# Optimization experiments

Hardware: AMD Instinct MI355X
Metric: run time of the kernel (lower is better)

## Reference

```python
import jax, jax.numpy as jnp
import numpy as np

B, N, D, L = 32, 512, 768, 4  # batch, nodes (incl. CLS at last index), in_dim==hidden_size, num_layers


def setup_inputs() -> dict:
    key = jax.random.key(0)
    ks = jax.random.split(key, 6)
    feature = jax.random.normal(ks[0], (B, N, D), jnp.float32)
    # token mask: random valid lengths, CLS node at the last index always present
    lengths = jax.random.randint(ks[1], (B,), N // 2, N)
    pmask = (jnp.arange(N)[None, :] < lengths[:, None]).astype(jnp.float32)
    pmask = pmask.at[:, -1].set(1.0)
    # L2C (learning-to-connect) bilinear gate params, one pair per layer
    Wq = jax.random.normal(ks[2], (L, D, D), jnp.float32) / np.sqrt(D)
    Wk = jax.random.normal(ks[3], (L, D, D), jnp.float32) / np.sqrt(D)
    # attention-pool projection Linear(in_dim, 1)
    proj_w = jax.random.normal(ks[4], (D,), jnp.float32) / np.sqrt(D)
    proj_b = jnp.zeros((), jnp.float32)
    return dict(pmask=pmask, feature=feature, Wq=Wq, Wk=Wk, proj_w=proj_w, proj_b=proj_b)


def reference(pmask, feature, Wq, Wk, proj_w, proj_b):
    full_adj = pmask[:, :, None] * pmask[:, None, :]        # [B,N,N]
    full_sum = jnp.sum(full_adj) + 1e-8
    p_sum = pmask.sum(-1)                                    # [B]
    scale = 1.0 / np.sqrt(D)
    preds = [feature]
    adjs, c_list, g_list = [], [], []
    total_l0 = jnp.zeros((), feature.dtype)
    for l in range(L):
        # L2C: bilinear sigmoid gate masked by full adjacency, L0-style loss = mean gate mass
        q = jnp.einsum('bnd,de->bne', feature, Wq[l])
        k = jnp.einsum('bnd,de->bne', feature, Wk[l])
        adj = jax.nn.sigmoid(jnp.einsum('bne,bme->bnm', q, k) * scale) * full_adj  # [B,N,N]
        total_l0 = total_l0 + jnp.sum(adj) / full_sum
        # sparse_statistics: CLS-row sparsity and graph-edge sparsity
        c_list.append(adj[:, -1, :-1].sum(-1) / p_sum)               # [B]
        g_list.append(adj[:, :-1, :-1].sum((-1, -2)) / p_sum ** 2)   # [B]
        adjs.append(adj)
        # symmetric degree normalization: D^-1/2 A D^-1/2 (diag bmm == row/col scaling)
        deg = adj.sum(2)                                              # [B,N]
        dis = jnp.where(deg > 0, jax.lax.rsqrt(jnp.maximum(deg, 1e-12)), 0.0)
        dis = jax.lax.stop_gradient(dis)                              # .detach() in original
        adj_n = dis[:, :, None] * adj * dis[:, None, :]
        # feature = adj_^T @ feature
        feature = jnp.einsum('bnm,bnd->bmd', adj_n, feature)
        preds.append(feature)
    pps = jnp.stack(preds, axis=2)                                    # [B,N,L+1,D]
    retain = jax.nn.sigmoid(jnp.einsum('bnld,d->bnl', pps, proj_w) + proj_b)  # [B,N,L+1]
    out = jnp.einsum('bnl,bnld->bnd', retain, pps)                    # [B,N,D]
    c_sparsity = jnp.stack(c_list, axis=-1)                           # [B,L]
    g_sparsity = jnp.stack(g_list, axis=-1)                           # [B,L]
    return (out, retain, jnp.stack(adjs, axis=-1), total_l0 / L, c_sparsity, g_sparsity)
```

## Files before the change

### kernel.cpp

```cpp
#include <hip/hip_runtime.h>

typedef short s16x8 __attribute__((ext_vector_type(8)));
typedef float f32x4 __attribute__((ext_vector_type(4)));

constexpr int BATCH = 32, NODES = 512, DIM = 768, LAYERS = 4;
constexpr float QK_SCALE = 0.03608439182435161f;

constexpr size_t OUT_OFF  = 0;
constexpr size_t RET_OFF  = (size_t)BATCH * NODES * DIM;
constexpr size_t ADJS_OFF = RET_OFF + (size_t)BATCH * NODES * (LAYERS + 1);
constexpr size_t L0_OFF   = ADJS_OFF + (size_t)BATCH * NODES * NODES * LAYERS;
constexpr size_t C_OFF    = L0_OFF + 1;
constexpr size_t G_OFF    = C_OFF + BATCH * LAYERS;

#define DEVI static __device__ __forceinline__

DEVI float bf2f(unsigned short u) {
    union { unsigned int i; float f; } v; v.i = ((unsigned int)u) << 16; return v.f;
}
DEVI unsigned short f2bf(float f) {
    union { float f; unsigned int i; } v; v.f = f;
    return (unsigned short)((v.i + 0x7FFFu + ((v.i >> 16) & 1u)) >> 16);
}
DEVI ushort4 pk4(float4 v) {
    ushort4 o; o.x = f2bf(v.x); o.y = f2bf(v.y); o.z = f2bf(v.z); o.w = f2bf(v.w); return o;
}
DEVI float sigm(float x) { return 1.0f / (1.0f + __expf(-x)); }
DEVI float deg2dis(float d) { return d > 0.f ? rsqrtf(fmaxf(d, 1e-12f)) : 0.f; }

DEVI void gload16(const unsigned short* g, unsigned short* l) {
    __builtin_amdgcn_global_load_lds(
        (const __attribute__((address_space(1))) unsigned int*)g,
        (__attribute__((address_space(3))) unsigned int*)l, 16, 0, 0);
}

template <int MODE>
__global__ __launch_bounds__(256) void gemm_nt(
    const unsigned short* __restrict__ A0, const unsigned short* __restrict__ Bq,
    const unsigned short* __restrict__ Bk, unsigned short* __restrict__ C0,
    int K, int lda, int ldb, int ldc,
    long sA, long sB, long sC,
    const float* __restrict__ pmask, float* __restrict__ deg,
    unsigned short* __restrict__ adjT,
    float* __restrict__ l0_acc, float* __restrict__ c_acc, float* __restrict__ g_acc,
    int layer)
{
    __shared__ __align__(16) unsigned short As[128 * 32];
    __shared__ __align__(16) unsigned short Bs[128 * 32];
    __shared__ float pmr[128];
    __shared__ float pmc[128];

    const int tid  = threadIdx.x;
    const int lane = tid & 63;
    const int wave = tid >> 6;
    const int wr = (wave >> 1) << 6;
    const int wc = (wave & 1) << 6;
    const int z = blockIdx.z;
    const int rows0 = blockIdx.x << 7;
    const int cols0 = blockIdx.y << 7;

    const unsigned short* A = A0 + (size_t)z * sA + (size_t)rows0 * lda;
    const unsigned short* Bsrc = ((MODE == 0 && z == 1) ? Bk : Bq) + (size_t)z * sB + (size_t)cols0 * ldb;

    f32x4 acc[4][4] = {};

    const int srow = wave * 16 + (lane >> 2);
    const int scb  = (lane & 3) << 3;
    const unsigned short* Ag = A + (size_t)srow * lda + scb;
    const unsigned short* Bg = Bsrc + (size_t)srow * ldb + scb;
    unsigned short* lA0 = &As[wave * 512];
    unsigned short* lA1 = &As[2048 + wave * 512];
    unsigned short* lB0 = &Bs[wave * 512];
    unsigned short* lB1 = &Bs[2048 + wave * 512];
    const size_t a64 = (size_t)64 * lda, b64 = (size_t)64 * ldb;

    const int mrow = lane & 15;
    const int kq   = (lane >> 4) << 3;

    for (int kt = 0; kt < K; kt += 32) {
        __syncthreads();
        gload16(Ag + kt, lA0);
        gload16(Ag + a64 + kt, lA1);
        gload16(Bg + kt, lB0);
        gload16(Bg + b64 + kt, lB1);
        __syncthreads();

        s16x8 af[4], bfr[4];
        #pragma unroll
        for (int i = 0; i < 4; ++i) {
            af[i]  = *(const s16x8*)(&As[(wr + i * 16 + mrow) * 32 + kq]);
            bfr[i] = *(const s16x8*)(&Bs[(wc + i * 16 + mrow) * 32 + kq]);
        }
        #pragma unroll
        for (int i = 0; i < 4; ++i)
            #pragma unroll
            for (int j = 0; j < 4; ++j)
                acc[i][j] = __builtin_amdgcn_mfma_f32_16x16x32_bf16(af[i], bfr[j], acc[i][j], 0, 0, 0);
    }

    const int colb = lane & 15, quad = lane >> 4;

    if constexpr (MODE != 1) {
        unsigned short* C = C0 + (size_t)z * sC;
        #pragma unroll
        for (int i = 0; i < 4; ++i) {
            const int rbase = rows0 + wr + i * 16 + (quad << 2);
            float dv[4];
            if constexpr (MODE == 2) {
                #pragma unroll
                for (int r = 0; r < 4; ++r) dv[r] = deg2dis(deg[(size_t)z * NODES + rbase + r]);
            }
            #pragma unroll
            for (int j = 0; j < 4; ++j) {
                const int cc = cols0 + wc + j * 16 + colb;
                #pragma unroll
                for (int r = 0; r < 4; ++r) {
                    float v = acc[i][j][r];
                    if constexpr (MODE == 2) v *= dv[r];
                    C[(size_t)(rbase + r) * ldc + cc] = f2bf(v);
                }
            }
        }
    } else {
        __syncthreads();
        if (tid < 128) pmr[tid] = pmask[(size_t)z * NODES + rows0 + tid];
        else if (tid < 256) pmc[tid - 128] = pmask[(size_t)z * NODES + cols0 + (tid - 128)];
        __syncthreads();

        float tot = 0.f, gs = 0.f, cs = 0.f;
        #pragma unroll
        for (int i = 0; i < 4; ++i) {
            const int nloc = wr + i * 16 + (quad << 2);
            #pragma unroll
            for (int r = 0; r < 4; ++r) {
                const int n = rows0 + nloc + r;
                const float pmn = pmr[nloc + r];
                float dp = 0.f;
                #pragma unroll
                for (int j = 0; j < 4; ++j) {
                    const int mloc = wc + j * 16 + colb;
                    const int m = cols0 + mloc;
                    float a = pmn * pmc[mloc] * sigm(acc[i][j][r] * QK_SCALE);
                    acc[i][j][r] = a;
                    dp += a;
                    tot += a;
                    if (m < NODES - 1) {
                        if (n < NODES - 1) gs += a;
                        else cs += a;
                    }
                }
                dp += __shfl_xor(dp, 1, 16);
                dp += __shfl_xor(dp, 2, 16);
                dp += __shfl_xor(dp, 4, 16);
                dp += __shfl_xor(dp, 8, 16);
                if (colb == 0) atomicAdd(&deg[(size_t)z * NODES + n], dp);
            }
        }
        #pragma unroll
        for (int i = 0; i < 4; ++i) {
            const int nb = rows0 + wr + i * 16 + (quad << 2);
            #pragma unroll
            for (int j = 0; j < 4; ++j) {
                const int m = cols0 + wc + j * 16 + colb;
                ushort4 pk;
                pk.x = f2bf(acc[i][j][0]); pk.y = f2bf(acc[i][j][1]);
                pk.z = f2bf(acc[i][j][2]); pk.w = f2bf(acc[i][j][3]);
                *(ushort4*)(adjT + ((size_t)z * NODES + m) * NODES + nb) = pk;
            }
        }
        #pragma unroll
        for (int o = 1; o < 64; o <<= 1) {
            tot += __shfl_xor(tot, o, 64);
            gs  += __shfl_xor(gs, o, 64);
            cs  += __shfl_xor(cs, o, 64);
        }
        if (lane == 0) {
            atomicAdd(l0_acc, tot);
            atomicAdd(&g_acc[z * LAYERS + layer], gs);
            atomicAdd(&c_acc[z * LAYERS + layer], cs);
        }
    }
}

__global__ __launch_bounds__(256) void interleave_adjs(
    const unsigned short* __restrict__ adjT, float* __restrict__ adjs)
{
    __shared__ unsigned short t[4][32][36];
    const int b = blockIdx.z, m0 = blockIdx.x << 5, n0 = blockIdx.y << 5;
    const int tr = threadIdx.x >> 3, tc = (threadIdx.x & 7) << 2;
    #pragma unroll
    for (int l = 0; l < LAYERS; ++l) {
        ushort4 v = *(const ushort4*)(adjT + (((size_t)l * BATCH + b) * NODES + m0 + tr) * NODES + n0 + tc);
        t[l][tr][tc] = v.x; t[l][tr][tc + 1] = v.y; t[l][tr][tc + 2] = v.z; t[l][tr][tc + 3] = v.w;
    }
    __syncthreads();
    float* dst = adjs + (((size_t)b * NODES + n0 + tr) * NODES + m0 + tc) * LAYERS;
    #pragma unroll
    for (int mm = 0; mm < 4; ++mm) {
        float4 f;
        f.x = bf2f(t[0][tc + mm][tr]); f.y = bf2f(t[1][tc + mm][tr]);
        f.z = bf2f(t[2][tc + mm][tr]); f.w = bf2f(t[3][tc + mm][tr]);
        *(float4*)(dst + mm * 4) = f;
    }
}

__global__ void transpose_w(const float* __restrict__ Wq, const float* __restrict__ Wk,
                            unsigned short* __restrict__ Wqt, unsigned short* __restrict__ Wkt)
{
    __shared__ unsigned short t[32][36];
    const int which = blockIdx.z >> 2, l = blockIdx.z & 3;
    const float* src = (which ? Wk : Wq) + (size_t)l * DIM * DIM;
    unsigned short* dst = (which ? Wkt : Wqt) + (size_t)l * DIM * DIM;
    const int r0 = blockIdx.x << 5, c0 = blockIdx.y << 5;
    const int tr = threadIdx.x >> 3, tc = (threadIdx.x & 7) << 2;
    float4 v = *(const float4*)(src + (size_t)(r0 + tr) * DIM + c0 + tc);
    t[tr][tc] = f2bf(v.x); t[tr][tc + 1] = f2bf(v.y);
    t[tr][tc + 2] = f2bf(v.z); t[tr][tc + 3] = f2bf(v.w);
    __syncthreads();
    ushort4 o;
    o.x = t[tc + 0][tr]; o.y = t[tc + 1][tr]; o.z = t[tc + 2][tr]; o.w = t[tc + 3][tr];
    *(ushort4*)(dst + (size_t)(c0 + tr) * DIM + r0 + tc) = o;
}

__global__ void fp_transpose(const unsigned short* __restrict__ X, const float* __restrict__ deg,
                             unsigned short* __restrict__ fpt)
{
    __shared__ unsigned short t[32][36];
    const int b = blockIdx.z;
    const int n0 = blockIdx.x << 5, d0 = blockIdx.y << 5;
    const int tr = threadIdx.x >> 3, tc = (threadIdx.x & 7) << 2;
    const float dv = deg2dis(deg[(size_t)b * NODES + n0 + tr]);
    ushort4 v = *(const ushort4*)(X + ((size_t)b * NODES + n0 + tr) * DIM + d0 + tc);
    t[tr][tc]     = f2bf(bf2f(v.x) * dv);
    t[tr][tc + 1] = f2bf(bf2f(v.y) * dv);
    t[tr][tc + 2] = f2bf(bf2f(v.z) * dv);
    t[tr][tc + 3] = f2bf(bf2f(v.w) * dv);
    __syncthreads();
    ushort4 o;
    o.x = t[tc + 0][tr]; o.y = t[tc + 1][tr]; o.z = t[tc + 2][tr]; o.w = t[tc + 3][tr];
    *(ushort4*)(fpt + ((size_t)b * DIM + d0 + tr) * NODES + n0 + tc) = o;
}

__global__ void f2bf_kernel(const float* __restrict__ x, unsigned short* __restrict__ y)
{
    const size_t i = ((size_t)blockIdx.x * 256 + threadIdx.x) << 2;
    float4 v = *(const float4*)(x + i);
    *(ushort4*)(y + i) = pk4(v);
}

__global__ void psum_kernel(const float* __restrict__ pm, float* __restrict__ ps)
{
    const int b = blockIdx.x, t = threadIdx.x;
    float s = pm[(size_t)b * NODES + t] + pm[(size_t)b * NODES + 256 + t];
    #pragma unroll
    for (int o = 1; o < 64; o <<= 1) s += __shfl_xor(s, o, 64);
    __shared__ float sh[4];
    if ((t & 63) == 0) sh[t >> 6] = s;
    __syncthreads();
    if (t == 0) ps[b] = sh[0] + sh[1] + sh[2] + sh[3];
}

__global__ __launch_bounds__(256) void final_out(
    const float* __restrict__ X0f, const unsigned short* __restrict__ X1,
    const unsigned short* __restrict__ X2, const unsigned short* __restrict__ X3,
    const unsigned short* __restrict__ X4,
    const float* __restrict__ pw, const float* __restrict__ pb,
    const float* __restrict__ ps, const float* __restrict__ c_acc,
    const float* __restrict__ g_acc, const float* __restrict__ l0,
    float* __restrict__ ob)
{
    if (blockIdx.x == 0) {
        const int t = threadIdx.x;
        if (t < BATCH * LAYERS) {
            const int b = t >> 2;
            const float p = ps[b];
            ob[C_OFF + t] = c_acc[t] / p;
            ob[G_OFF + t] = g_acc[t] / (p * p);
        }
        if (t == 0) {
            float fs = 1e-8f;
            for (int b = 0; b < BATCH; ++b) fs += ps[b] * ps[b];
            ob[L0_OFF] = l0[0] / (fs * (float)LAYERS);
        }
    }

    const int row = (blockIdx.x << 2) + (threadIdx.x >> 6);
    const int lane = threadIdx.x & 63;
    const unsigned short* Xb[4] = { X1 + (size_t)row * DIM, X2 + (size_t)row * DIM,
                                    X3 + (size_t)row * DIM, X4 + (size_t)row * DIM };
    float xs[5][12];
    float dot[5] = {};
    #pragma unroll
    for (int c = 0; c < 3; ++c) {
        const int idx = c * 256 + (lane << 2);
        float4 wv = *(const float4*)(pw + idx);
        float4 x0 = *(const float4*)(X0f + (size_t)row * DIM + idx);
        xs[0][c * 4 + 0] = x0.x; xs[0][c * 4 + 1] = x0.y;
        xs[0][c * 4 + 2] = x0.z; xs[0][c * 4 + 3] = x0.w;
        dot[0] += x0.x * wv.x + x0.y * wv.y + x0.z * wv.z + x0.w * wv.w;
        #pragma unroll
        for (int l = 0; l < 4; ++l) {
            ushort4 xv = *(const ushort4*)(Xb[l] + idx);
            float a0 = bf2f(xv.x), a1 = bf2f(xv.y), a2 = bf2f(xv.z), a3 = bf2f(xv.w);
            xs[l + 1][c * 4 + 0] = a0; xs[l + 1][c * 4 + 1] = a1;
            xs[l + 1][c * 4 + 2] = a2; xs[l + 1][c * 4 + 3] = a3;
            dot[l + 1] += a0 * wv.x + a1 * wv.y + a2 * wv.z + a3 * wv.w;
        }
    }
    #pragma unroll
    for (int l = 0; l < 5; ++l)
        #pragma unroll
        for (int o = 1; o < 64; o <<= 1) dot[l] += __shfl_xor(dot[l], o, 64);
    const float pbv = pb[0];
    float r[5];
    #pragma unroll
    for (int l = 0; l < 5; ++l) r[l] = sigm(dot[l] + pbv);
    if (lane == 0) {
        float* rr = ob + RET_OFF + (size_t)row * (LAYERS + 1);
        rr[0] = r[0]; rr[1] = r[1]; rr[2] = r[2]; rr[3] = r[3]; rr[4] = r[4];
    }
    float* orow = ob + OUT_OFF + (size_t)row * DIM;
    #pragma unroll
    for (int c = 0; c < 3; ++c) {
        float4 p;
        p.x = r[0] * xs[0][c * 4 + 0]; p.y = r[0] * xs[0][c * 4 + 1];
        p.z = r[0] * xs[0][c * 4 + 2]; p.w = r[0] * xs[0][c * 4 + 3];
        #pragma unroll
        for (int l = 1; l < 5; ++l) {
            p.x += r[l] * xs[l][c * 4 + 0]; p.y += r[l] * xs[l][c * 4 + 1];
            p.z += r[l] * xs[l][c * 4 + 2]; p.w += r[l] * xs[l][c * 4 + 3];
        }
        *(float4*)(orow + c * 256 + (lane << 2)) = p;
    }
}

extern "C" void kernel_launch(void* const* d_in, const int* in_sizes, int n_in,
                              void* d_out, int out_size, void* d_ws, size_t ws_size,
                              hipStream_t stream)
{
    (void)in_sizes; (void)n_in; (void)out_size; (void)ws_size;
    const float* pmask = (const float*)d_in[0];
    const float* feat  = (const float*)d_in[1];
    const float* Wq    = (const float*)d_in[2];
    const float* Wk    = (const float*)d_in[3];
    const float* projw = (const float*)d_in[4];
    const float* projb = (const float*)d_in[5];
    float* ob = (float*)d_out;

    char* w = (char*)d_ws;
    unsigned short* Xb[4];
    Xb[0] = (unsigned short*)(w + 0);
    Xb[1] = (unsigned short*)(w + 25165824);
    Xb[2] = (unsigned short*)(w + 50331648);
    Xb[3] = (unsigned short*)(w + 75497472);
    unsigned short* qws   = (unsigned short*)(w + 100663296);
    unsigned short* kws   = (unsigned short*)(w + 125829120);
    unsigned short* featb = (unsigned short*)(w + 150994944);
    unsigned short* adjT  = (unsigned short*)(w + 176160768);
    unsigned short* Wqt   = (unsigned short*)(w + 243269632);
    unsigned short* Wkt   = (unsigned short*)(w + 247988224);
    float* deg_all = (float*)(w + 252706816);
    float* c_acc   = (float*)(w + 252968960);
    float* g_acc   = (float*)(w + 252969472);
    float* l0_acc  = (float*)(w + 252969984);
    float* p_sum   = (float*)(w + 252970240);

    dim3 blk(256);
    hipMemsetAsync(w + 252706816, 0, 263680, stream);

    f2bf_kernel<<<dim3(12288), blk, 0, stream>>>(feat, featb);
    transpose_w<<<dim3(24, 24, 8), blk, 0, stream>>>(Wq, Wk, Wqt, Wkt);
    psum_kernel<<<dim3(32), blk, 0, stream>>>(pmask, p_sum);

    for (int l = 0; l < LAYERS; ++l) {
        float* deg_l = deg_all + (size_t)l * BATCH * NODES;
        unsigned short* adjT_l = adjT + (size_t)l * BATCH * NODES * NODES;
        const unsigned short* Xsrc = (l == 0) ? featb : Xb[l - 1];

        gemm_nt<0><<<dim3(128, 6, 2), blk, 0, stream>>>(
            Xsrc, Wqt + (size_t)l * DIM * DIM, Wkt + (size_t)l * DIM * DIM, qws,
            DIM, DIM, DIM, DIM, 0L, 0L, (long)BATCH * NODES * DIM,
            nullptr, nullptr, nullptr, nullptr, nullptr, nullptr, 0);

        gemm_nt<1><<<dim3(4, 4, 32), blk, 0, stream>>>(
            qws, kws, nullptr, nullptr,
            DIM, DIM, DIM, 0, (long)NODES * DIM, (long)NODES * DIM, 0L,
            pmask, deg_l, adjT_l, l0_acc, c_acc, g_acc, l);

        fp_transpose<<<dim3(16, 24, 32), blk, 0, stream>>>(Xsrc, deg_l, qws);

        gemm_nt<2><<<dim3(4, 6, 32), blk, 0, stream>>>(
            adjT_l, qws, nullptr, Xb[l],
            NODES, NODES, NODES, DIM, (long)NODES * NODES, (long)DIM * NODES, (long)NODES * DIM,
            nullptr, deg_l, nullptr, nullptr, nullptr, nullptr, 0);
    }

    interleave_adjs<<<dim3(16, 16, 32), blk, 0, stream>>>(adjT, ob + ADJS_OFF);
    final_out<<<dim3(4096), blk, 0, stream>>>(feat, Xb[0], Xb[1], Xb[2], Xb[3],
                                              projw, projb, p_sum, c_acc, g_acc, l0_acc, ob);
}
```

Before: 915.0 us.

## Fold Wq·Wkᵀ into one matrix per layer to drop the K projection GEMM

Precomputes M = Wq·Wkᵀ for each layer with a small batched GEMM. Each layer then runs a single projection X·M, and the score GEMM uses X directly as the key operand. This halves the per-layer projection GEMM work and removes the k workspace and the weight-transpose kernel. It also merges the feature and weight casts into one launch. Rounding M to bf16 changes numerics slightly.

```diff
diff --git a/kernel.cpp b/kernel.cpp
--- a/kernel.cpp
+++ b/kernel.cpp
@@ -36,8 +36,8 @@
 
 template <int MODE>
 __global__ __launch_bounds__(256) void gemm_nt(
-    const unsigned short* __restrict__ A0, const unsigned short* __restrict__ Bq,
-    const unsigned short* __restrict__ Bk, unsigned short* __restrict__ C0,
+    const unsigned short* __restrict__ A0, const unsigned short* __restrict__ B0,
+    unsigned short* __restrict__ C0,
     int K, int lda, int ldb, int ldc,
     long sA, long sB, long sC,
     const float* __restrict__ pmask, float* __restrict__ deg,
@@ -60,7 +60,7 @@
     const int cols0 = blockIdx.y << 7;
 
     const unsigned short* A = A0 + (size_t)z * sA + (size_t)rows0 * lda;
-    const unsigned short* Bsrc = ((MODE == 0 && z == 1) ? Bk : Bq) + (size_t)z * sB + (size_t)cols0 * ldb;
+    const unsigned short* Bsrc = B0 + (size_t)z * sB + (size_t)cols0 * ldb;
 
     f32x4 acc[4][4] = {};
 
@@ -204,24 +204,6 @@
     }
 }
 
-__global__ void transpose_w(const float* __restrict__ Wq, const float* __restrict__ Wk,
-                            unsigned short* __restrict__ Wqt, unsigned short* __restrict__ Wkt)
-{
-    __shared__ unsigned short t[32][36];
-    const int which = blockIdx.z >> 2, l = blockIdx.z & 3;
-    const float* src = (which ? Wk : Wq) + (size_t)l * DIM * DIM;
-    unsigned short* dst = (which ? Wkt : Wqt) + (size_t)l * DIM * DIM;
-    const int r0 = blockIdx.x << 5, c0 = blockIdx.y << 5;
-    const int tr = threadIdx.x >> 3, tc = (threadIdx.x & 7) << 2;
-    float4 v = *(const float4*)(src + (size_t)(r0 + tr) * DIM + c0 + tc);
-    t[tr][tc] = f2bf(v.x); t[tr][tc + 1] = f2bf(v.y);
-    t[tr][tc + 2] = f2bf(v.z); t[tr][tc + 3] = f2bf(v.w);
-    __syncthreads();
-    ushort4 o;
-    o.x = t[tc + 0][tr]; o.y = t[tc + 1][tr]; o.z = t[tc + 2][tr]; o.w = t[tc + 3][tr];
-    *(ushort4*)(dst + (size_t)(c0 + tr) * DIM + r0 + tc) = o;
-}
-
 __global__ void fp_transpose(const unsigned short* __restrict__ X, const float* __restrict__ deg,
                              unsigned short* __restrict__ fpt)
 {
@@ -241,11 +223,18 @@
     *(ushort4*)(fpt + ((size_t)b * DIM + d0 + tr) * NODES + n0 + tc) = o;
 }
 
-__global__ void f2bf_kernel(const float* __restrict__ x, unsigned short* __restrict__ y)
-{
-    const size_t i = ((size_t)blockIdx.x * 256 + threadIdx.x) << 2;
-    float4 v = *(const float4*)(x + i);
-    *(ushort4*)(y + i) = pk4(v);
+__global__ void cast_all(const float* __restrict__ feat, const float* __restrict__ Wq,
+                         const float* __restrict__ Wk, unsigned short* __restrict__ featb,
+                         unsigned short* __restrict__ Wqb, unsigned short* __restrict__ Wkb)
+{
+    const int bx = blockIdx.x;
+    const float* src; unsigned short* dst; size_t base;
+    if (bx < 12288)      { src = feat; dst = featb; base = (size_t)bx * 1024; }
+    else if (bx < 14592) { src = Wq;   dst = Wqb;   base = (size_t)(bx - 12288) * 1024; }
+    else                 { src = Wk;   dst = Wkb;   base = (size_t)(bx - 14592) * 1024; }
+    const size_t i = base + ((size_t)threadIdx.x << 2);
+    float4 v = *(const float4*)(src + i);
+    *(ushort4*)(dst + i) = pk4(v);
 }
 
 __global__ void psum_kernel(const float* __restrict__ pm, float* __restrict__ ps)
@@ -354,43 +343,47 @@
     Xb[2] = (unsigned short*)(w + 50331648);
     Xb[3] = (unsigned short*)(w + 75497472);
     unsigned short* qws   = (unsigned short*)(w + 100663296);
-    unsigned short* kws   = (unsigned short*)(w + 125829120);
-    unsigned short* featb = (unsigned short*)(w + 150994944);
-    unsigned short* adjT  = (unsigned short*)(w + 176160768);
-    unsigned short* Wqt   = (unsigned short*)(w + 243269632);
-    unsigned short* Wkt   = (unsigned short*)(w + 247988224);
-    float* deg_all = (float*)(w + 252706816);
-    float* c_acc   = (float*)(w + 252968960);
-    float* g_acc   = (float*)(w + 252969472);
-    float* l0_acc  = (float*)(w + 252969984);
-    float* p_sum   = (float*)(w + 252970240);
+    unsigned short* featb = (unsigned short*)(w + 125829120);
+    unsigned short* adjT  = (unsigned short*)(w + 150994944);
+    unsigned short* Wqb   = (unsigned short*)(w + 218103808);
+    unsigned short* Wkb   = (unsigned short*)(w + 222822400);
+    unsigned short* MT    = (unsigned short*)(w + 227540992);
+    float* deg_all = (float*)(w + 232259584);
+    float* c_acc   = (float*)(w + 232521728);
+    float* g_acc   = (float*)(w + 232522240);
+    float* l0_acc  = (float*)(w + 232522752);
+    float* p_sum   = (float*)(w + 232523008);
 
     dim3 blk(256);
-    hipMemsetAsync(w + 252706816, 0, 263680, stream);
-
-    f2bf_kernel<<<dim3(12288), blk, 0, stream>>>(feat, featb);
-    transpose_w<<<dim3(24, 24, 8), blk, 0, stream>>>(Wq, Wk, Wqt, Wkt);
+    hipMemsetAsync(w + 232259584, 0, 263680, stream);
+
+    cast_all<<<dim3(16896), blk, 0, stream>>>(feat, Wq, Wk, featb, Wqb, Wkb);
     psum_kernel<<<dim3(32), blk, 0, stream>>>(pmask, p_sum);
+
+    gemm_nt<0><<<dim3(6, 6, 4), blk, 0, stream>>>(
+        Wkb, Wqb, MT, DIM, DIM, DIM, DIM,
+        (long)DIM * DIM, (long)DIM * DIM, (long)DIM * DIM,
+        nullptr, nullptr, nullptr, nullptr, nullptr, nullptr, 0);
 
     for (int l = 0; l < LAYERS; ++l) {
         float* deg_l = deg_all + (size_t)l * BATCH * NODES;
         unsigned short* adjT_l = adjT + (size_t)l * BATCH * NODES * NODES;
         const unsigned short* Xsrc = (l == 0) ? featb : Xb[l - 1];
 
-        gemm_nt<0><<<dim3(128, 6, 2), blk, 0, stream>>>(
-            Xsrc, Wqt + (size_t)l * DIM * DIM, Wkt + (size_t)l * DIM * DIM, qws,
-            DIM, DIM, DIM, DIM, 0L, 0L, (long)BATCH * NODES * DIM,
+        gemm_nt<0><<<dim3(128, 6, 1), blk, 0, stream>>>(
+            Xsrc, MT + (size_t)l * DIM * DIM, qws,
+            DIM, DIM, DIM, DIM, 0L, 0L, 0L,
             nullptr, nullptr, nullptr, nullptr, nullptr, nullptr, 0);
 
         gemm_nt<1><<<dim3(4, 4, 32), blk, 0, stream>>>(
-            qws, kws, nullptr, nullptr,
+            qws, Xsrc, nullptr,
             DIM, DIM, DIM, 0, (long)NODES * DIM, (long)NODES * DIM, 0L,
             pmask, deg_l, adjT_l, l0_acc, c_acc, g_acc, l);
 
         fp_transpose<<<dim3(16, 24, 32), blk, 0, stream>>>(Xsrc, deg_l, qws);
 
         gemm_nt<2><<<dim3(4, 6, 32), blk, 0, stream>>>(
-            adjT_l, qws, nullptr, Xb[l],
+            adjT_l, qws, Xb[l],
             NODES, NODES, NODES, DIM, (long)NODES * NODES, (long)DIM * NODES, (long)NODES * DIM,
             nullptr, deg_l, nullptr, nullptr, nullptr, nullptr, 0);
     }
```

Measured after the change: 838.7 us. 8.3% less time.
